# Performance work log

Hardware: AMD Instinct MI355X
Metric: run time of the kernel (lower is better)

## Reference

```python
import jax, jax.numpy as jnp
import numpy as np

S = 4096          # number of samples
N_NODES = 2048    # sum nodes in this layer
N_CHILD = 4096    # nodes per child layer
NNZ = 32768       # nonzeros per sparse log-weight matrix


def setup_inputs() -> dict:
    key = jax.random.key(0)
    ks = jax.random.split(key, 8)
    ll0 = jax.random.normal(ks[0], (S, N_CHILD), dtype=jnp.float32)
    ll1 = jax.random.normal(ks[1], (S, N_CHILD), dtype=jnp.float32)
    w0_data = jax.random.normal(ks[2], (NNZ,), dtype=jnp.float32)
    w1_data = jax.random.normal(ks[3], (NNZ,), dtype=jnp.float32)
    w0_rows = jax.random.randint(ks[4], (NNZ,), 0, N_NODES, dtype=jnp.int32)
    w0_cols = jax.random.randint(ks[5], (NNZ,), 0, N_CHILD, dtype=jnp.int32)
    w1_rows = jax.random.randint(ks[6], (NNZ,), 0, N_NODES, dtype=jnp.int32)
    w1_cols = jax.random.randint(ks[7], (NNZ,), 0, N_CHILD, dtype=jnp.int32)
    return {"ll0": ll0, "ll1": ll1,
            "w0_data": w0_data, "w1_data": w1_data,
            "w0_rows": w0_rows, "w0_cols": w0_cols,
            "w1_rows": w1_rows, "w1_cols": w1_cols,
            "n_nodes": N_NODES}


def _sparse_weighted_sum(ll, data, rows, cols, n_nodes):
    # exp(ll) @ exp(W).T for BCOO W with shape (n_nodes, n_child)
    # contrib[s, k] = exp(ll[s, cols[k]]) * exp(data[k]); scatter-add over rows.
    contrib = jnp.exp(ll[:, cols] + data[None, :])  # (S, NNZ)
    return jnp.zeros((ll.shape[0], n_nodes), dtype=ll.dtype).at[:, rows].add(contrib)


def reference(ll0, ll1, w0_data, w1_data, w0_rows, w0_cols, w1_rows, w1_cols, n_nodes):
    # accumulate exp(ll_i) @ exp(W_i).T over child layers
    result = _sparse_weighted_sum(ll0, w0_data, w0_rows, w0_cols, n_nodes)
    result = result + _sparse_weighted_sum(ll1, w1_data, w1_rows, w1_cols, n_nodes)
    # log normalization constants: log(sum_j exp(concatenated log_weights)[i, j])
    z = jnp.zeros((n_nodes,), dtype=result.dtype)
    z = z.at[w0_rows].add(jnp.exp(w0_data))
    z = z.at[w1_rows].add(jnp.exp(w1_data))
    return jnp.log(result) - jnp.log(z)[None, :]
```

## Files before the change

kernel.cpp:

```cpp
#include <hip/hip_runtime.h>
#include <math.h>

#define S 4096
#define N_NODES 2048
#define N_CHILD 4096
#define NNZ 32768
#define NNZ_TOTAL (2 * NNZ)
#define TSM 512
#define TN 8
#define CAP 96
#define LP 516

typedef float f32x2 __attribute__((ext_vector_type(2)));


__global__ __launch_bounds__(256) void scatter_kernel(
        const float* __restrict__ w0d, const float* __restrict__ w1d,
        const int* __restrict__ w0r, const int* __restrict__ w0c,
        const int* __restrict__ w1r, const int* __restrict__ w1c,
        int2* __restrict__ ent, int* __restrict__ counts) {
    int k = blockIdx.x * 256 + threadIdx.x;
    int row, col; float w;
    if (k < NNZ) { row = w0r[k]; col = w0c[k]; w = w0d[k]; }
    else { int kk = k - NNZ; row = w1r[kk]; col = w1c[kk] + N_CHILD; w = w1d[kk]; }
    int pos = atomicAdd(&counts[row], 1);
    if (pos < CAP)
        ent[row * CAP + pos] = make_int2(col, __float_as_int(__expf(w)));
}

__global__ __launch_bounds__(256, 8) void texp_kernel(
        const float* __restrict__ ll0, const float* __restrict__ ll1,
        unsigned char* __restrict__ ET) {
    __shared__ unsigned int tile[256 * 5];
    int t = threadIdx.x, wave = t >> 6, lane = t & 63;
    int bt = blockIdx.x;
    int slice = bt & 7;
    int ssub = (bt >> 3) & 31;
    int ct = (bt >> 8) & 15;
    int z = (bt >> 12) & 1;
    int s0 = slice * 512 + ssub * 16;
    int c0 = ct * 256;
    const float* ll = z ? ll1 : ll0;
    const float* p = ll + (size_t)(s0 + wave * 4) * N_CHILD + c0 + lane * 4;
    float4 a0 = *(const float4*)(p);
    float4 a1 = *(const float4*)(p + N_CHILD);
    float4 a2 = *(const float4*)(p + 2 * N_CHILD);
    float4 a3 = *(const float4*)(p + 3 * N_CHILD);
#pragma unroll
    for (int k = 0; k < 4; ++k) {
        float e0 = __expf(((const float*)&a0)[k]);
        float e1 = __expf(((const float*)&a1)[k]);
        float e2 = __expf(((const float*)&a2)[k]);
        float e3 = __expf(((const float*)&a3)[k]);
        unsigned int wlo = (unsigned int)__builtin_amdgcn_cvt_pk_fp8_f32(
            e0, e1, 0, false);
        unsigned int wfull = (unsigned int)__builtin_amdgcn_cvt_pk_fp8_f32(
            e2, e3, (int)wlo, true);
        tile[(k * 64 + lane) * 5 + wave] = wfull;
    }
    __syncthreads();
    unsigned int d0 = tile[t * 5 + 0];
    unsigned int d1 = tile[t * 5 + 1];
    unsigned int d2 = tile[t * 5 + 2];
    unsigned int d3 = tile[t * 5 + 3];
    int c = (t & 63) * 4 + (t >> 6);
    unsigned char* dst = ET + (size_t)(z * N_CHILD + c0 + c) * S + s0;
    *(uint4*)dst = make_uint4(d0, d1, d2, d3);
}


static __device__ inline void fma16(uint4 x, float w, float* a) {
#pragma unroll
    for (int q = 0; q < 4; ++q) {
        unsigned int word = (q == 0) ? x.x : (q == 1) ? x.y : (q == 2) ? x.z : x.w;
        f32x2 lo = __builtin_amdgcn_cvt_pk_f32_fp8(word, false);
        f32x2 hi = __builtin_amdgcn_cvt_pk_f32_fp8(word, true);
        a[q * 4 + 0] = fmaf(lo.x, w, a[q * 4 + 0]);
        a[q * 4 + 1] = fmaf(lo.y, w, a[q * 4 + 1]);
        a[q * 4 + 2] = fmaf(hi.x, w, a[q * 4 + 2]);
        a[q * 4 + 3] = fmaf(hi.y, w, a[q * 4 + 3]);
    }
}

__global__ __launch_bounds__(256, 8) void main_kernel(
        const unsigned char* __restrict__ ET, const int2* __restrict__ ent,
        const int* __restrict__ counts, float* __restrict__ out) {
    __shared__ float lds[TN * LP];
    int t = threadIdx.x, wave = t >> 6, lane = t & 63;
    int hs = lane >> 5, sl = lane & 31;
    int slice = blockIdx.x & 7;
    int nb = blockIdx.x >> 3;
    int i0 = nb * TN;
    const unsigned char* ETs = ET + slice * TSM + sl * 16;
    for (int jj = 0; jj < 2; ++jj) {
        int j = wave * 2 + jj;
        int i = i0 + j;
        int cnt = __builtin_amdgcn_readfirstlane(counts[i]);
        if (cnt > CAP) cnt = CAP;
        const int2* eb = ent + i * CAP;
        float a[16];
#pragma unroll
        for (int u = 0; u < 16; ++u) a[u] = 0.f;
        float z = 0.f;
        int n = (cnt + 1 - hs) >> 1;
        int t2 = 0;
        for (; t2 + 1 < n; t2 += 2) {
            int2 e0 = eb[hs + 2 * t2];
            int2 e1 = eb[hs + 2 * t2 + 2];
            uint4 x0 = *(const uint4*)(ETs + (size_t)e0.x * S);
            uint4 x1 = *(const uint4*)(ETs + (size_t)e1.x * S);
            float w0 = __uint_as_float(e0.y);
            float w1 = __uint_as_float(e1.y);
            fma16(x0, w0, a);
            fma16(x1, w1, a);
            z += w0 + w1;
        }
        if (t2 < n) {
            int2 e0 = eb[hs + 2 * t2];
            uint4 x0 = *(const uint4*)(ETs + (size_t)e0.x * S);
            float w0 = __uint_as_float(e0.y);
            fma16(x0, w0, a);
            z += w0;
        }
#pragma unroll
        for (int u = 0; u < 16; ++u) a[u] += __shfl_xor(a[u], 32);
        z += __shfl_xor(z, 32);
        float lz = __logf(z);
        float r[8];
#pragma unroll
        for (int u = 0; u < 8; ++u) r[u] = __logf(a[hs * 8 + u]) - lz;
        float* dstl = &lds[j * LP + sl * 16 + hs * 8];
        *(float4*)(dstl)     = make_float4(r[0], r[1], r[2], r[3]);
        *(float4*)(dstl + 4) = make_float4(r[4], r[5], r[6], r[7]);
    }
    __syncthreads();
    float* obase = out + (size_t)slice * TSM * N_NODES + i0;
#pragma unroll
    for (int q = 0; q < 8; ++q) {
        int elem = (t + 256 * q) * 2;
        int s_l = elem >> 3;
        int i_l = elem & 7;
        float2 v;
        v.x = lds[i_l * LP + s_l];
        v.y = lds[(i_l + 1) * LP + s_l];
        *(float2*)&obase[(size_t)s_l * N_NODES + i_l] = v;
    }
}


extern "C" void kernel_launch(void* const* d_in, const int* in_sizes, int n_in,
                              void* d_out, int out_size, void* d_ws, size_t ws_size,
                              hipStream_t stream) {
    const float* ll0 = (const float*)d_in[0];
    const float* ll1 = (const float*)d_in[1];
    const float* w0d = (const float*)d_in[2];
    const float* w1d = (const float*)d_in[3];
    const int*   w0r = (const int*)d_in[4];
    const int*   w0c = (const int*)d_in[5];
    const int*   w1r = (const int*)d_in[6];
    const int*   w1c = (const int*)d_in[7];
    float* out = (float*)d_out;

    unsigned char* ET = (unsigned char*)d_ws;
    int2* ent   = (int2*)(ET + (size_t)2 * N_CHILD * S);
    int*  counts = (int*)(ent + (size_t)N_NODES * CAP);

    hipMemsetAsync(counts, 0, sizeof(int) * N_NODES, stream);
    scatter_kernel<<<256, 256, 0, stream>>>(w0d, w1d, w0r, w0c, w1r, w1c,
                                            ent, counts);
    texp_kernel<<<8192, 256, 0, stream>>>(ll0, ll1, ET);
    main_kernel<<<(N_NODES / TN) * (S / TSM), 256, 0, stream>>>(ET, ent, counts, out);
}
```

Before: 225.1 us.

## Merge scatter and transpose-exp kernels into one launch; use packed f32x2 FMAs

The sparse-entry scatter kernel and the transposed fp8 exp kernel are merged into a single prep kernel launch, with the first 256 blocks doing the scatter and the rest doing the transpose. This removes one kernel launch and lets the two independent prep stages run concurrently. Separately, the main kernel's FMA accumulation is rewritten on 2-wide float vectors so the compiler can emit packed FMA instructions, halving the FMA instruction count in the inner loop. The hs-dependent accumulator selection becomes a per-element select, which may add a few instructions.

```diff
diff --git a/kernel.cpp b/kernel.cpp
--- a/kernel.cpp
+++ b/kernel.cpp
@@ -14,26 +14,27 @@
 typedef float f32x2 __attribute__((ext_vector_type(2)));
 
 
-__global__ __launch_bounds__(256) void scatter_kernel(
+__global__ __launch_bounds__(256, 8) void prep_kernel(
+        const float* __restrict__ ll0, const float* __restrict__ ll1,
         const float* __restrict__ w0d, const float* __restrict__ w1d,
         const int* __restrict__ w0r, const int* __restrict__ w0c,
         const int* __restrict__ w1r, const int* __restrict__ w1c,
-        int2* __restrict__ ent, int* __restrict__ counts) {
-    int k = blockIdx.x * 256 + threadIdx.x;
-    int row, col; float w;
-    if (k < NNZ) { row = w0r[k]; col = w0c[k]; w = w0d[k]; }
-    else { int kk = k - NNZ; row = w1r[kk]; col = w1c[kk] + N_CHILD; w = w1d[kk]; }
-    int pos = atomicAdd(&counts[row], 1);
-    if (pos < CAP)
-        ent[row * CAP + pos] = make_int2(col, __float_as_int(__expf(w)));
-}
-
-__global__ __launch_bounds__(256, 8) void texp_kernel(
-        const float* __restrict__ ll0, const float* __restrict__ ll1,
-        unsigned char* __restrict__ ET) {
+        unsigned char* __restrict__ ET, int2* __restrict__ ent,
+        int* __restrict__ counts) {
     __shared__ unsigned int tile[256 * 5];
-    int t = threadIdx.x, wave = t >> 6, lane = t & 63;
-    int bt = blockIdx.x;
+    int t = threadIdx.x;
+    int b = blockIdx.x;
+    if (b < 256) {
+        int k = b * 256 + t;
+        int row, col; float w;
+        if (k < NNZ) { row = w0r[k]; col = w0c[k]; w = w0d[k]; }
+        else { int kk = k - NNZ; row = w1r[kk]; col = w1c[kk] + N_CHILD; w = w1d[kk]; }
+        int pos = atomicAdd(&counts[row], 1);
+        if (pos < CAP)
+            ent[row * CAP + pos] = make_int2(col, __float_as_int(__expf(w)));
+        return;
+    }
+    int bt = b - 256;
     int slice = bt & 7;
     int ssub = (bt >> 3) & 31;
     int ct = (bt >> 8) & 15;
@@ -41,6 +42,7 @@
     int s0 = slice * 512 + ssub * 16;
     int c0 = ct * 256;
     const float* ll = z ? ll1 : ll0;
+    int wave = t >> 6, lane = t & 63;
     const float* p = ll + (size_t)(s0 + wave * 4) * N_CHILD + c0 + lane * 4;
     float4 a0 = *(const float4*)(p);
     float4 a1 = *(const float4*)(p + N_CHILD);
@@ -69,16 +71,14 @@
 }
 
 
-static __device__ inline void fma16(uint4 x, float w, float* a) {
+static __device__ inline void fma16(uint4 x, f32x2 w2, f32x2* a2) {
 #pragma unroll
     for (int q = 0; q < 4; ++q) {
         unsigned int word = (q == 0) ? x.x : (q == 1) ? x.y : (q == 2) ? x.z : x.w;
         f32x2 lo = __builtin_amdgcn_cvt_pk_f32_fp8(word, false);
         f32x2 hi = __builtin_amdgcn_cvt_pk_f32_fp8(word, true);
-        a[q * 4 + 0] = fmaf(lo.x, w, a[q * 4 + 0]);
-        a[q * 4 + 1] = fmaf(lo.y, w, a[q * 4 + 1]);
-        a[q * 4 + 2] = fmaf(hi.x, w, a[q * 4 + 2]);
-        a[q * 4 + 3] = fmaf(hi.y, w, a[q * 4 + 3]);
+        a2[q * 2 + 0] = lo * w2 + a2[q * 2 + 0];
+        a2[q * 2 + 1] = hi * w2 + a2[q * 2 + 1];
     }
 }
 
@@ -98,9 +98,9 @@
         int cnt = __builtin_amdgcn_readfirstlane(counts[i]);
         if (cnt > CAP) cnt = CAP;
         const int2* eb = ent + i * CAP;
-        float a[16];
+        f32x2 a2[8];
 #pragma unroll
-        for (int u = 0; u < 16; ++u) a[u] = 0.f;
+        for (int u = 0; u < 8; ++u) a2[u] = (f32x2){0.f, 0.f};
         float z = 0.f;
         int n = (cnt + 1 - hs) >> 1;
         int t2 = 0;
@@ -111,24 +111,33 @@
             uint4 x1 = *(const uint4*)(ETs + (size_t)e1.x * S);
             float w0 = __uint_as_float(e0.y);
             float w1 = __uint_as_float(e1.y);
-            fma16(x0, w0, a);
-            fma16(x1, w1, a);
+            f32x2 w02 = {w0, w0};
+            f32x2 w12 = {w1, w1};
+            fma16(x0, w02, a2);
+            fma16(x1, w12, a2);
             z += w0 + w1;
         }
         if (t2 < n) {
             int2 e0 = eb[hs + 2 * t2];
             uint4 x0 = *(const uint4*)(ETs + (size_t)e0.x * S);
             float w0 = __uint_as_float(e0.y);
-            fma16(x0, w0, a);
+            f32x2 w02 = {w0, w0};
+            fma16(x0, w02, a2);
             z += w0;
         }
+        float fl[16];
 #pragma unroll
-        for (int u = 0; u < 16; ++u) a[u] += __shfl_xor(a[u], 32);
+        for (int u = 0; u < 8; ++u) { fl[2 * u] = a2[u].x; fl[2 * u + 1] = a2[u].y; }
+#pragma unroll
+        for (int u = 0; u < 16; ++u) fl[u] += __shfl_xor(fl[u], 32);
         z += __shfl_xor(z, 32);
         float lz = __logf(z);
         float r[8];
 #pragma unroll
-        for (int u = 0; u < 8; ++u) r[u] = __logf(a[hs * 8 + u]) - lz;
+        for (int u = 0; u < 8; ++u) {
+            float sel = hs ? fl[8 + u] : fl[u];
+            r[u] = __logf(sel) - lz;
+        }
         float* dstl = &lds[j * LP + sl * 16 + hs * 8];
         *(float4*)(dstl)     = make_float4(r[0], r[1], r[2], r[3]);
         *(float4*)(dstl + 4) = make_float4(r[4], r[5], r[6], r[7]);
@@ -166,8 +175,7 @@
     int*  counts = (int*)(ent + (size_t)N_NODES * CAP);
 
     hipMemsetAsync(counts, 0, sizeof(int) * N_NODES, stream);
-    scatter_kernel<<<256, 256, 0, stream>>>(w0d, w1d, w0r, w0c, w1r, w1c,
-                                            ent, counts);
-    texp_kernel<<<8192, 256, 0, stream>>>(ll0, ll1, ET);
+    prep_kernel<<<256 + 8192, 256, 0, stream>>>(ll0, ll1, w0d, w1d, w0r, w0c,
+                                                w1r, w1c, ET, ent, counts);
     main_kernel<<<(N_NODES / TN) * (S / TSM), 256, 0, stream>>>(ET, ent, counts, out);
 }
```

Measured after the change: 225.5 us. About the same (+0.2%).
